# Kernel optimization log

Measured on AMD Instinct MI355X. Metric: run time of the kernel, lower is better.

The kernel has to match this reference:

```python
import jax, jax.numpy as jnp
import numpy as np
import math

B, C, H, W = 16, 256, 128, 128
N = 4096
D = 256  # out_channels
IMG = 512


def _bilinear_sample(features, grid):
    """features (B,C,H,W), grid (B,N,2) in [-1,1] (x,y). align_corners=True, border padding."""
    Bq, Cq, Hq, Wq = features.shape
    ix = (grid[..., 0] + 1.0) * 0.5 * (Wq - 1)  # (B,N)
    iy = (grid[..., 1] + 1.0) * 0.5 * (Hq - 1)
    # border padding: clamp continuous coords into valid range
    ix = jnp.clip(ix, 0.0, Wq - 1)
    iy = jnp.clip(iy, 0.0, Hq - 1)
    x0 = jnp.floor(ix)
    y0 = jnp.floor(iy)
    wx = ix - x0
    wy = iy - y0
    x0i = jnp.clip(x0.astype(jnp.int32), 0, Wq - 1)
    y0i = jnp.clip(y0.astype(jnp.int32), 0, Hq - 1)
    x1i = jnp.clip(x0i + 1, 0, Wq - 1)
    y1i = jnp.clip(y0i + 1, 0, Hq - 1)
    f = features.reshape(Bq, Cq, Hq * Wq)

    def gather(yi, xi):
        idx = (yi * Wq + xi)[:, None, :]  # (B,1,N)
        return jnp.take_along_axis(f, idx, axis=2)  # (B,C,N)

    v00 = gather(y0i, x0i)
    v01 = gather(y0i, x1i)
    v10 = gather(y1i, x0i)
    v11 = gather(y1i, x1i)
    wx = wx[:, None, :]
    wy = wy[:, None, :]
    top = v00 * (1 - wx) + v01 * wx
    bot = v10 * (1 - wx) + v11 * wx
    return top * (1 - wy) + bot * wy  # (B,C,N)


def _pos_encoding(positions, d_model):
    """positions (B,N,2) in [0,1] -> (B,N,2*d_model) sinusoidal."""
    div_term = jnp.exp(jnp.arange(0, d_model, 2, dtype=jnp.float32)
                       * (-math.log(10000.0) / d_model))  # (d_model//2,)
    x = positions[..., 0:1] * 1000.0  # (B,N,1)
    y = positions[..., 1:2] * 1000.0

    def interleave(v):
        a = v * div_term  # (B,N,d_model//2)
        sc = jnp.stack([jnp.sin(a), jnp.cos(a)], axis=-1)  # (B,N,d//2,2)
        return sc.reshape(*v.shape[:-1], d_model)

    return jnp.concatenate([interleave(x), interleave(y)], axis=-1)


def setup_inputs() -> dict:
    key = jax.random.key(0)
    ks = jax.random.split(key, 8)
    features = jax.random.normal(ks[0], (B, C, H, W), dtype=jnp.float32)
    vertices = jax.random.uniform(ks[1], (B, N, 2), dtype=jnp.float32) * IMG
    s1 = 1.0 / math.sqrt(C)
    s2 = 1.0 / math.sqrt(D)
    W1 = jax.random.uniform(ks[2], (C, D), jnp.float32, -s1, s1)
    b1 = jnp.zeros((D,), jnp.float32)
    W2 = jax.random.uniform(ks[3], (D, D), jnp.float32, -s2, s2)
    b2 = jnp.zeros((D,), jnp.float32)
    Wp = jax.random.uniform(ks[4], (D, D), jnp.float32, -s2, s2)
    bp = jnp.zeros((D,), jnp.float32)
    return {"features": features, "vertices": vertices, "image_size": IMG,
            "W1": W1, "b1": b1, "W2": W2, "b2": b2, "Wp": Wp, "bp": bp}


def reference(features, vertices, image_size, W1, b1, W2, b2, Wp, bp):
    # normalize pixel coords to [-1,1] (align_corners=True convention)
    denom = jnp.float32(image_size - 1)
    grid = 2.0 * vertices / denom - 1.0  # (B,N,2)
    sampled = _bilinear_sample(features, grid)  # (B,C,N)
    sampled = jnp.transpose(sampled, (0, 2, 1))  # (B,N,C)
    h = jax.nn.relu(jnp.einsum('bnc,cd->bnd', sampled, W1) + b1)
    vfeat = jnp.einsum('bnd,de->bne', h, W2) + b2  # (B,N,D)
    pos_enc = _pos_encoding(vertices / jnp.float32(image_size), D // 2)  # (B,N,D)
    out = jnp.einsum('bnd,de->bne', vfeat + pos_enc, Wp) + bp
    return out
```

## Files before the change

### kernel.cpp

```cpp
#include <hip/hip_runtime.h>

#define HW 16384
#define Nn 4096

typedef __bf16 bf16x8 __attribute__((ext_vector_type(8)));
typedef unsigned short us8t __attribute__((ext_vector_type(8)));
typedef float f32x4 __attribute__((ext_vector_type(4)));

__device__ __forceinline__ unsigned short f2bf(float f) {
    unsigned int u = __float_as_uint(f);
    u = (u + 0x7fffu + ((u >> 16) & 1u)) >> 16;
    return (unsigned short)u;
}
__device__ __forceinline__ float bf2f(unsigned int h) {
    return __uint_as_float(h << 16);
}
__device__ __forceinline__ f32x4 mfma16(us8t a, us8t b, f32x4 c) {
    return __builtin_amdgcn_mfma_f32_16x16x32_bf16(
        __builtin_bit_cast(bf16x8, a), __builtin_bit_cast(bf16x8, b), c, 0, 0, 0);
}

__global__ __launch_bounds__(256) void k_wt(const float* __restrict__ W1,
                                            const float* __restrict__ W2,
                                            const float* __restrict__ Wp,
                                            unsigned short* __restrict__ WT) {
    const int m = blockIdx.x >> 8;
    const int d = blockIdx.x & 255;
    const int c = threadIdx.x;
    const float* W = (m == 0) ? W1 : (m == 1) ? W2 : Wp;
    WT[m * 65536 + d * 256 + c] = f2bf(W[c * 256 + d]);
}

__global__ __launch_bounds__(256) void k_gemm1(const float* __restrict__ f,
                                               const unsigned short* __restrict__ W1T,
                                               unsigned short* __restrict__ S, int b0) {
    __shared__ __align__(16) unsigned short Asb[64][40];

    const int blk = blockIdx.x;
    const int bl = blk >> 8;
    const int b = b0 + bl;
    const int p0 = (blk & 255) << 6;
    const int t = threadIdx.x;
    const int lane = t & 63;
    const int w = t >> 6;
    const int sc = t >> 4;
    const int sp = (t & 15) << 2;
    const int mrow = lane & 15;
    const int kg = (lane >> 4) << 3;
    const int n0w = w << 6;

    const float* fb = f + ((size_t)b << 22);

    f32x4 acc[4][4];
#pragma unroll
    for (int i = 0; i < 4; ++i)
#pragma unroll
        for (int j = 0; j < 4; ++j) acc[i][j] = (f32x4){0.f, 0.f, 0.f, 0.f};

    us8t bnx[4];
#pragma unroll
    for (int nt = 0; nt < 4; ++nt)
        bnx[nt] = *(const us8t*)(W1T + ((n0w + (nt << 4) + mrow) << 8) + kg);

    for (int k0 = 0; k0 < 256; k0 += 32) {
        __syncthreads();
#pragma unroll
        for (int it = 0; it < 2; ++it) {
            const int c = sc + (it << 4);
            const float4 v = *(const float4*)(fb + ((size_t)(k0 + c) << 14) + p0 + sp);
            Asb[sp + 0][c] = f2bf(v.x);
            Asb[sp + 1][c] = f2bf(v.y);
            Asb[sp + 2][c] = f2bf(v.z);
            Asb[sp + 3][c] = f2bf(v.w);
        }
        us8t bcur[4];
#pragma unroll
        for (int nt = 0; nt < 4; ++nt) bcur[nt] = bnx[nt];
        if (k0 < 224) {
#pragma unroll
            for (int nt = 0; nt < 4; ++nt)
                bnx[nt] = *(const us8t*)(W1T + ((n0w + (nt << 4) + mrow) << 8) + k0 + 32 + kg);
        }
        __syncthreads();
        us8t af[4];
#pragma unroll
        for (int mt = 0; mt < 4; ++mt)
            af[mt] = *(const us8t*)&Asb[(mt << 4) + mrow][kg];
#pragma unroll
        for (int mt = 0; mt < 4; ++mt)
#pragma unroll
            for (int nt = 0; nt < 4; ++nt)
                acc[mt][nt] = mfma16(af[mt], bcur[nt], acc[mt][nt]);
    }

    unsigned short* Sp = S + ((((size_t)bl << 14) + p0) << 8);
    const int r0 = (lane >> 4) << 2;
#pragma unroll
    for (int mt = 0; mt < 4; ++mt)
#pragma unroll
        for (int nt = 0; nt < 4; ++nt) {
            const int col = n0w + (nt << 4) + mrow;
#pragma unroll
            for (int j = 0; j < 4; ++j) {
                const int row = (mt << 4) + r0 + j;
                Sp[((size_t)row << 8) + col] = f2bf(acc[mt][nt][j]);
            }
        }
}

__global__ __launch_bounds__(256) void k_fused(const unsigned short* __restrict__ S,
                                               const float* __restrict__ verts,
                                               const int* __restrict__ iszp,
                                               const unsigned short* __restrict__ W2T,
                                               const unsigned short* __restrict__ WpT,
                                               const float* __restrict__ b1,
                                               const float* __restrict__ b2,
                                               const float* __restrict__ bpv,
                                               float* __restrict__ out, int b0) {
    __shared__ __align__(16) unsigned short hT[64][264];
    __shared__ __align__(16) int pIdx[64][4];
    __shared__ __align__(16) float wBl[64][4];
    __shared__ float vps[64][2];
    __shared__ __align__(16) float b1s[256];
    __shared__ float b2s[256], bps[256];

    const int blk = blockIdx.x;
    const int bl = blk >> 6;
    const int b = b0 + bl;
    const int n0 = (blk & 63) << 6;
    const int t = threadIdx.x;
    const int lane = t & 63;
    const int w = t >> 6;

    b1s[t] = b1[t];
    b2s[t] = b2[t];
    bps[t] = bpv[t];

    if (t < 64) {
        const float isz = (float)iszp[0];
        const size_t vo = ((size_t)b * Nn + n0 + t) << 1;
        const float vx = verts[vo + 0];
        const float vy = verts[vo + 1];
        const float gs = 127.0f / (isz - 1.0f);
        const float ix = fminf(fmaxf(vx * gs, 0.0f), 127.0f);
        const float iy = fminf(fmaxf(vy * gs, 0.0f), 127.0f);
        const float x0 = floorf(ix), y0 = floorf(iy);
        const float wx = ix - x0, wy = iy - y0;
        const int x0i = (int)x0, y0i = (int)y0;
        const int x1i = min(x0i + 1, 127), y1i = min(y0i + 1, 127);
        pIdx[t][0] = (y0i << 7) + x0i;
        pIdx[t][1] = (y0i << 7) + x1i;
        pIdx[t][2] = (y1i << 7) + x0i;
        pIdx[t][3] = (y1i << 7) + x1i;
        wBl[t][0] = (1.0f - wx) * (1.0f - wy);
        wBl[t][1] = wx * (1.0f - wy);
        wBl[t][2] = (1.0f - wx) * wy;
        wBl[t][3] = wx * wy;
        vps[t][0] = vx / isz;
        vps[t][1] = vy / isz;
    }
    __syncthreads();

    {
        const unsigned short* Sb = S + ((size_t)bl << 22);
        const float4 bl1 = *(const float4*)&b1s[lane << 2];
        for (int i = 0; i < 16; ++i) {
            const int r = (w << 4) + i;
            const int4 pp = *(const int4*)pIdx[r];
            const float4 wt = *(const float4*)wBl[r];
            const uint2 a0 = *(const uint2*)(Sb + ((size_t)pp.x << 8) + (lane << 2));
            const uint2 a1 = *(const uint2*)(Sb + ((size_t)pp.y << 8) + (lane << 2));
            const uint2 a2 = *(const uint2*)(Sb + ((size_t)pp.z << 8) + (lane << 2));
            const uint2 a3 = *(const uint2*)(Sb + ((size_t)pp.w << 8) + (lane << 2));
            float d0 = wt.x * bf2f(a0.x & 0xffffu) + wt.y * bf2f(a1.x & 0xffffu) +
                       wt.z * bf2f(a2.x & 0xffffu) + wt.w * bf2f(a3.x & 0xffffu) + bl1.x;
            float d1 = wt.x * bf2f(a0.x >> 16) + wt.y * bf2f(a1.x >> 16) +
                       wt.z * bf2f(a2.x >> 16) + wt.w * bf2f(a3.x >> 16) + bl1.y;
            float d2 = wt.x * bf2f(a0.y & 0xffffu) + wt.y * bf2f(a1.y & 0xffffu) +
                       wt.z * bf2f(a2.y & 0xffffu) + wt.w * bf2f(a3.y & 0xffffu) + bl1.z;
            float d3 = wt.x * bf2f(a0.y >> 16) + wt.y * bf2f(a1.y >> 16) +
                       wt.z * bf2f(a2.y >> 16) + wt.w * bf2f(a3.y >> 16) + bl1.w;
            d0 = fmaxf(d0, 0.0f);
            d1 = fmaxf(d1, 0.0f);
            d2 = fmaxf(d2, 0.0f);
            d3 = fmaxf(d3, 0.0f);
            uint2 pk;
            pk.x = (unsigned)f2bf(d0) | ((unsigned)f2bf(d1) << 16);
            pk.y = (unsigned)f2bf(d2) | ((unsigned)f2bf(d3) << 16);
            *(uint2*)&hT[r][lane << 2] = pk;
        }
    }
    __syncthreads();

    const int mrow = lane & 15;
    const int kg = (lane >> 4) << 3;
    const int r0 = (lane >> 4) << 2;
    const int n0w = w << 6;

    f32x4 acc[4][4];
#pragma unroll
    for (int i = 0; i < 4; ++i)
#pragma unroll
        for (int j = 0; j < 4; ++j) acc[i][j] = (f32x4){0.f, 0.f, 0.f, 0.f};

    us8t bnx[4];
#pragma unroll
    for (int nt = 0; nt < 4; ++nt)
        bnx[nt] = *(const us8t*)(W2T + ((n0w + (nt << 4) + mrow) << 8) + kg);
    for (int k0 = 0; k0 < 256; k0 += 32) {
        us8t bcur[4];
#pragma unroll
        for (int nt = 0; nt < 4; ++nt) bcur[nt] = bnx[nt];
        if (k0 < 224) {
#pragma unroll
            for (int nt = 0; nt < 4; ++nt)
                bnx[nt] = *(const us8t*)(W2T + ((n0w + (nt << 4) + mrow) << 8) + k0 + 32 + kg);
        }
        us8t af[4];
#pragma unroll
        for (int mt = 0; mt < 4; ++mt)
            af[mt] = *(const us8t*)&hT[(mt << 4) + mrow][k0 + kg];
#pragma unroll
        for (int mt = 0; mt < 4; ++mt)
#pragma unroll
            for (int nt = 0; nt < 4; ++nt)
                acc[mt][nt] = mfma16(af[mt], bcur[nt], acc[mt][nt]);
    }
    __syncthreads();

    const float C2 = -0.20762050593046f;
#pragma unroll
    for (int nt = 0; nt < 4; ++nt) {
        const int col = n0w + (nt << 4) + mrow;
        const float bias2 = b2s[col];
        const int ci = col & 127;
        const float dv = exp2f((float)(ci >> 1) * C2) * 1000.0f;
        const int sel = col >> 7;
#pragma unroll
        for (int mt = 0; mt < 4; ++mt)
#pragma unroll
            for (int j = 0; j < 4; ++j) {
                const int row = (mt << 4) + r0 + j;
                const float ang = vps[row][sel] * dv;
                const float pe = (col & 1) ? __cosf(ang) : __sinf(ang);
                hT[row][col] = f2bf(acc[mt][nt][j] + bias2 + pe);
            }
    }
    __syncthreads();

#pragma unroll
    for (int i = 0; i < 4; ++i)
#pragma unroll
        for (int j = 0; j < 4; ++j) acc[i][j] = (f32x4){0.f, 0.f, 0.f, 0.f};
#pragma unroll
    for (int nt = 0; nt < 4; ++nt)
        bnx[nt] = *(const us8t*)(WpT + ((n0w + (nt << 4) + mrow) << 8) + kg);
    for (int k0 = 0; k0 < 256; k0 += 32) {
        us8t bcur[4];
#pragma unroll
        for (int nt = 0; nt < 4; ++nt) bcur[nt] = bnx[nt];
        if (k0 < 224) {
#pragma unroll
            for (int nt = 0; nt < 4; ++nt)
                bnx[nt] = *(const us8t*)(WpT + ((n0w + (nt << 4) + mrow) << 8) + k0 + 32 + kg);
        }
        us8t af[4];
#pragma unroll
        for (int mt = 0; mt < 4; ++mt)
            af[mt] = *(const us8t*)&hT[(mt << 4) + mrow][k0 + kg];
#pragma unroll
        for (int mt = 0; mt < 4; ++mt)
#pragma unroll
            for (int nt = 0; nt < 4; ++nt)
                acc[mt][nt] = mfma16(af[mt], bcur[nt], acc[mt][nt]);
    }

    float* ob = out + (((size_t)b * Nn + n0) << 8);
#pragma unroll
    for (int nt = 0; nt < 4; ++nt) {
        const int col = n0w + (nt << 4) + mrow;
        const float bb = bps[col];
#pragma unroll
        for (int mt = 0; mt < 4; ++mt)
#pragma unroll
            for (int j = 0; j < 4; ++j) {
                const int row = (mt << 4) + r0 + j;
                ob[((size_t)row << 8) + col] = acc[mt][nt][j] + bb;
            }
    }
}

extern "C" void kernel_launch(void* const* d_in, const int* in_sizes, int n_in,
                              void* d_out, int out_size, void* d_ws, size_t ws_size,
                              hipStream_t stream) {
    const float* f = (const float*)d_in[0];
    const float* verts = (const float*)d_in[1];
    const int* isz = (const int*)d_in[2];
    const float* W1 = (const float*)d_in[3];
    const float* b1 = (const float*)d_in[4];
    const float* W2 = (const float*)d_in[5];
    const float* b2 = (const float*)d_in[6];
    const float* Wp = (const float*)d_in[7];
    const float* bp = (const float*)d_in[8];
    float* out = (float*)d_out;

    unsigned short* WT = (unsigned short*)d_ws;
    const size_t S_OFF = 512u << 10;
    unsigned short* S = (unsigned short*)((char*)d_ws + S_OFF);

    const size_t perBatch = (size_t)HW * 256 * 2;
    size_t sbytes = (ws_size > S_OFF) ? (ws_size - S_OFF) : 0;
    int nbMax = (int)(sbytes / perBatch);
    if (nbMax < 1) nbMax = 1;
    if (nbMax > 16) nbMax = 16;

    k_wt<<<dim3(768), dim3(256), 0, stream>>>(W1, W2, Wp, WT);
    for (int b0 = 0; b0 < 16; b0 += nbMax) {
        const int nb = (16 - b0 < nbMax) ? (16 - b0) : nbMax;
        k_gemm1<<<dim3(nb * 256), dim3(256), 0, stream>>>(f, WT, S, b0);
        k_fused<<<dim3(nb * 64), dim3(256), 0, stream>>>(S, verts, isz, WT + 65536, WT + 131072,
                                                         b1, b2, bp, out, b0);
    }
}
```

Before: 515.5 us.

## Split gather from MLP kernel and load all channels up front in pixel GEMM

The pixel-projection GEMM now loads all 256 channels of a 64-pixel tile into LDS in one pass, using packed bf16 conversion, and drops the per-k-step barriers. It also swaps operand roles so the weights feed the MFMA A operand, which allows packed vector stores. The bilinear gather plus ReLU becomes its own kernel with one vertex per wave, writing h to a workspace buffer, and the MLP kernel reads h directly from global memory. This aims to raise gather parallelism and cut synchronisation, at the cost of an extra launch, an h round-trip through memory, and a smaller batch chunk per workspace.

```diff
diff --git a/kernel.cpp b/kernel.cpp
--- a/kernel.cpp
+++ b/kernel.cpp
@@ -6,6 +6,7 @@
 typedef __bf16 bf16x8 __attribute__((ext_vector_type(8)));
 typedef unsigned short us8t __attribute__((ext_vector_type(8)));
 typedef float f32x4 __attribute__((ext_vector_type(4)));
+typedef unsigned int u32x4 __attribute__((ext_vector_type(4)));
 
 __device__ __forceinline__ unsigned short f2bf(float f) {
     unsigned int u = __float_as_uint(f);
@@ -14,6 +15,11 @@
 }
 __device__ __forceinline__ float bf2f(unsigned int h) {
     return __uint_as_float(h << 16);
+}
+__device__ __forceinline__ unsigned int pack2bf(float lo, float hi) {
+    const unsigned int u0 = __float_as_uint(lo) + 0x8000u;
+    const unsigned int u1 = __float_as_uint(hi) + 0x8000u;
+    return __builtin_amdgcn_perm(u1, u0, 0x07060302u);
 }
 __device__ __forceinline__ f32x4 mfma16(us8t a, us8t b, f32x4 c) {
     return __builtin_amdgcn_mfma_f32_16x16x32_bf16(
@@ -31,10 +37,10 @@
     WT[m * 65536 + d * 256 + c] = f2bf(W[c * 256 + d]);
 }
 
-__global__ __launch_bounds__(256) void k_gemm1(const float* __restrict__ f,
-                                               const unsigned short* __restrict__ W1T,
-                                               unsigned short* __restrict__ S, int b0) {
-    __shared__ __align__(16) unsigned short Asb[64][40];
+__global__ __launch_bounds__(256) void k_pix(const float* __restrict__ f,
+                                             const unsigned short* __restrict__ W1T,
+                                             unsigned short* __restrict__ S, int b0) {
+    __shared__ __align__(16) unsigned int Asb[64 * 132];
 
     const int blk = blockIdx.x;
     const int bl = blk >> 8;
@@ -43,85 +49,145 @@
     const int t = threadIdx.x;
     const int lane = t & 63;
     const int w = t >> 6;
-    const int sc = t >> 4;
-    const int sp = (t & 15) << 2;
     const int mrow = lane & 15;
     const int kg = (lane >> 4) << 3;
-    const int n0w = w << 6;
 
     const float* fb = f + ((size_t)b << 22);
 
+    const int sp = (t & 15) << 2;
+    const int c8 = (t >> 4) << 3;
+#pragma unroll
+    for (int pass = 0; pass < 2; ++pass) {
+        const int c0 = c8 + (pass << 7);
+        f32x4 v[8];
+#pragma unroll
+        for (int i = 0; i < 8; ++i)
+            v[i] = *(const f32x4*)(fb + ((size_t)(c0 + i) << 14) + p0 + sp);
+#pragma unroll
+        for (int j = 0; j < 4; ++j) {
+            u32x4 pk;
+            pk.x = pack2bf(v[0][j], v[1][j]);
+            pk.y = pack2bf(v[2][j], v[3][j]);
+            pk.z = pack2bf(v[4][j], v[5][j]);
+            pk.w = pack2bf(v[6][j], v[7][j]);
+            *(u32x4*)&Asb[(sp + j) * 132 + (c0 >> 1)] = pk;
+        }
+    }
+
     f32x4 acc[4][4];
 #pragma unroll
     for (int i = 0; i < 4; ++i)
 #pragma unroll
         for (int j = 0; j < 4; ++j) acc[i][j] = (f32x4){0.f, 0.f, 0.f, 0.f};
 
-    us8t bnx[4];
-#pragma unroll
-    for (int nt = 0; nt < 4; ++nt)
-        bnx[nt] = *(const us8t*)(W1T + ((n0w + (nt << 4) + mrow) << 8) + kg);
-
+    const unsigned short* AW = W1T + (((w << 6) + mrow) << 8) + kg;
+    us8t aN[4];
+#pragma unroll
+    for (int mt = 0; mt < 4; ++mt) aN[mt] = *(const us8t*)(AW + (mt << 12));
+
+    __syncthreads();
+
+    const unsigned short* Bl = (const unsigned short*)Asb + mrow * 264 + kg;
+#pragma unroll
     for (int k0 = 0; k0 < 256; k0 += 32) {
-        __syncthreads();
-#pragma unroll
-        for (int it = 0; it < 2; ++it) {
-            const int c = sc + (it << 4);
-            const float4 v = *(const float4*)(fb + ((size_t)(k0 + c) << 14) + p0 + sp);
-            Asb[sp + 0][c] = f2bf(v.x);
-            Asb[sp + 1][c] = f2bf(v.y);
-            Asb[sp + 2][c] = f2bf(v.z);
-            Asb[sp + 3][c] = f2bf(v.w);
-        }
-        us8t bcur[4];
-#pragma unroll
-        for (int nt = 0; nt < 4; ++nt) bcur[nt] = bnx[nt];
+        us8t aC[4];
+#pragma unroll
+        for (int mt = 0; mt < 4; ++mt) aC[mt] = aN[mt];
         if (k0 < 224) {
 #pragma unroll
+            for (int mt = 0; mt < 4; ++mt)
+                aN[mt] = *(const us8t*)(AW + (mt << 12) + k0 + 32);
+        }
+        us8t bF[4];
+#pragma unroll
+        for (int nt = 0; nt < 4; ++nt)
+            bF[nt] = *(const us8t*)(Bl + nt * 16 * 264 + k0);
+#pragma unroll
+        for (int mt = 0; mt < 4; ++mt)
+#pragma unroll
             for (int nt = 0; nt < 4; ++nt)
-                bnx[nt] = *(const us8t*)(W1T + ((n0w + (nt << 4) + mrow) << 8) + k0 + 32 + kg);
-        }
-        __syncthreads();
-        us8t af[4];
-#pragma unroll
-        for (int mt = 0; mt < 4; ++mt)
-            af[mt] = *(const us8t*)&Asb[(mt << 4) + mrow][kg];
-#pragma unroll
-        for (int mt = 0; mt < 4; ++mt)
-#pragma unroll
-            for (int nt = 0; nt < 4; ++nt)
-                acc[mt][nt] = mfma16(af[mt], bcur[nt], acc[mt][nt]);
-    }
-
-    unsigned short* Sp = S + ((((size_t)bl << 14) + p0) << 8);
-    const int r0 = (lane >> 4) << 2;
-#pragma unroll
-    for (int mt = 0; mt < 4; ++mt)
-#pragma unroll
-        for (int nt = 0; nt < 4; ++nt) {
-            const int col = n0w + (nt << 4) + mrow;
-#pragma unroll
-            for (int j = 0; j < 4; ++j) {
-                const int row = (mt << 4) + r0 + j;
-                Sp[((size_t)row << 8) + col] = f2bf(acc[mt][nt][j]);
-            }
-        }
-}
-
-__global__ __launch_bounds__(256) void k_fused(const unsigned short* __restrict__ S,
-                                               const float* __restrict__ verts,
-                                               const int* __restrict__ iszp,
-                                               const unsigned short* __restrict__ W2T,
-                                               const unsigned short* __restrict__ WpT,
-                                               const float* __restrict__ b1,
-                                               const float* __restrict__ b2,
-                                               const float* __restrict__ bpv,
-                                               float* __restrict__ out, int b0) {
-    __shared__ __align__(16) unsigned short hT[64][264];
-    __shared__ __align__(16) int pIdx[64][4];
-    __shared__ __align__(16) float wBl[64][4];
+                acc[mt][nt] = mfma16(aC[mt], bF[nt], acc[mt][nt]);
+    }
+
+    unsigned short* Sp = S + ((((size_t)bl << 14) + p0 + mrow) << 8) + (w << 6) + ((lane >> 4) << 2);
+#pragma unroll
+    for (int nt = 0; nt < 4; ++nt) {
+        unsigned short* Sr = Sp + ((size_t)(nt << 4) << 8);
+#pragma unroll
+        for (int mt = 0; mt < 4; ++mt) {
+            uint2 pk;
+            pk.x = pack2bf(acc[mt][nt][0], acc[mt][nt][1]);
+            pk.y = pack2bf(acc[mt][nt][2], acc[mt][nt][3]);
+            *(uint2*)(Sr + (mt << 4)) = pk;
+        }
+    }
+}
+
+__global__ __launch_bounds__(256) void k_gather(const unsigned short* __restrict__ S,
+                                                const float* __restrict__ verts,
+                                                const int* __restrict__ iszp,
+                                                const float* __restrict__ b1,
+                                                unsigned short* __restrict__ h, int b0) {
+    const int t = threadIdx.x;
+    const int lane = t & 63;
+    const int w = t >> 6;
+    const int blk = blockIdx.x;
+    const int bl = blk >> 10;
+    const int n = ((blk & 1023) << 2) + w;
+    const int b = b0 + bl;
+
+    const float isz = (float)iszp[0];
+    const size_t vo = ((size_t)b * Nn + n) << 1;
+    const float vx = verts[vo];
+    const float vy = verts[vo + 1];
+    const float gs = 127.0f / (isz - 1.0f);
+    const float ix = fminf(fmaxf(vx * gs, 0.0f), 127.0f);
+    const float iy = fminf(fmaxf(vy * gs, 0.0f), 127.0f);
+    const float x0 = floorf(ix), y0 = floorf(iy);
+    const float wx = ix - x0, wy = iy - y0;
+    const int x0i = (int)x0, y0i = (int)y0;
+    const int x1i = min(x0i + 1, 127), y1i = min(y0i + 1, 127);
+    const float w00 = (1.0f - wx) * (1.0f - wy);
+    const float w01 = wx * (1.0f - wy);
+    const float w10 = (1.0f - wx) * wy;
+    const float w11 = wx * wy;
+
+    const unsigned short* Sb = S + ((size_t)bl << 22);
+    const int co = lane << 2;
+    const uint2 a0 = *(const uint2*)(Sb + (((size_t)(y0i << 7) + x0i) << 8) + co);
+    const uint2 a1 = *(const uint2*)(Sb + (((size_t)(y0i << 7) + x1i) << 8) + co);
+    const uint2 a2 = *(const uint2*)(Sb + (((size_t)(y1i << 7) + x0i) << 8) + co);
+    const uint2 a3 = *(const uint2*)(Sb + (((size_t)(y1i << 7) + x1i) << 8) + co);
+    const float4 bb = *(const float4*)(b1 + co);
+
+    float d0 = w00 * bf2f(a0.x & 0xffffu) + w01 * bf2f(a1.x & 0xffffu) +
+               w10 * bf2f(a2.x & 0xffffu) + w11 * bf2f(a3.x & 0xffffu) + bb.x;
+    float d1 = w00 * bf2f(a0.x >> 16) + w01 * bf2f(a1.x >> 16) +
+               w10 * bf2f(a2.x >> 16) + w11 * bf2f(a3.x >> 16) + bb.y;
+    float d2 = w00 * bf2f(a0.y & 0xffffu) + w01 * bf2f(a1.y & 0xffffu) +
+               w10 * bf2f(a2.y & 0xffffu) + w11 * bf2f(a3.y & 0xffffu) + bb.z;
+    float d3 = w00 * bf2f(a0.y >> 16) + w01 * bf2f(a1.y >> 16) +
+               w10 * bf2f(a2.y >> 16) + w11 * bf2f(a3.y >> 16) + bb.w;
+    d0 = fmaxf(d0, 0.0f);
+    d1 = fmaxf(d1, 0.0f);
+    d2 = fmaxf(d2, 0.0f);
+    d3 = fmaxf(d3, 0.0f);
+    uint2 pk;
+    pk.x = pack2bf(d0, d1);
+    pk.y = pack2bf(d2, d3);
+    *(uint2*)(h + (((size_t)bl * Nn + n) << 8) + co) = pk;
+}
+
+__global__ __launch_bounds__(256) void k_mlp(const unsigned short* __restrict__ h,
+                                             const float* __restrict__ verts,
+                                             const int* __restrict__ iszp,
+                                             const unsigned short* __restrict__ W2T,
+                                             const unsigned short* __restrict__ WpT,
+                                             const float* __restrict__ b2,
+                                             const float* __restrict__ bpv,
+                                             float* __restrict__ out, int b0) {
+    __shared__ __align__(16) unsigned short gT[64][264];
     __shared__ float vps[64][2];
-    __shared__ __align__(16) float b1s[256];
     __shared__ float b2s[256], bps[256];
 
     const int blk = blockIdx.x;
@@ -132,99 +198,49 @@
     const int lane = t & 63;
     const int w = t >> 6;
 
-    b1s[t] = b1[t];
     b2s[t] = b2[t];
     bps[t] = bpv[t];
-
     if (t < 64) {
         const float isz = (float)iszp[0];
         const size_t vo = ((size_t)b * Nn + n0 + t) << 1;
-        const float vx = verts[vo + 0];
-        const float vy = verts[vo + 1];
-        const float gs = 127.0f / (isz - 1.0f);
-        const float ix = fminf(fmaxf(vx * gs, 0.0f), 127.0f);
-        const float iy = fminf(fmaxf(vy * gs, 0.0f), 127.0f);
-        const float x0 = floorf(ix), y0 = floorf(iy);
-        const float wx = ix - x0, wy = iy - y0;
-        const int x0i = (int)x0, y0i = (int)y0;
-        const int x1i = min(x0i + 1, 127), y1i = min(y0i + 1, 127);
-        pIdx[t][0] = (y0i << 7) + x0i;
-        pIdx[t][1] = (y0i << 7) + x1i;
-        pIdx[t][2] = (y1i << 7) + x0i;
-        pIdx[t][3] = (y1i << 7) + x1i;
-        wBl[t][0] = (1.0f - wx) * (1.0f - wy);
-        wBl[t][1] = wx * (1.0f - wy);
-        wBl[t][2] = (1.0f - wx) * wy;
-        wBl[t][3] = wx * wy;
-        vps[t][0] = vx / isz;
-        vps[t][1] = vy / isz;
-    }
-    __syncthreads();
-
-    {
-        const unsigned short* Sb = S + ((size_t)bl << 22);
-        const float4 bl1 = *(const float4*)&b1s[lane << 2];
-        for (int i = 0; i < 16; ++i) {
-            const int r = (w << 4) + i;
-            const int4 pp = *(const int4*)pIdx[r];
-            const float4 wt = *(const float4*)wBl[r];
-            const uint2 a0 = *(const uint2*)(Sb + ((size_t)pp.x << 8) + (lane << 2));
-            const uint2 a1 = *(const uint2*)(Sb + ((size_t)pp.y << 8) + (lane << 2));
-            const uint2 a2 = *(const uint2*)(Sb + ((size_t)pp.z << 8) + (lane << 2));
-            const uint2 a3 = *(const uint2*)(Sb + ((size_t)pp.w << 8) + (lane << 2));
-            float d0 = wt.x * bf2f(a0.x & 0xffffu) + wt.y * bf2f(a1.x & 0xffffu) +
-                       wt.z * bf2f(a2.x & 0xffffu) + wt.w * bf2f(a3.x & 0xffffu) + bl1.x;
-            float d1 = wt.x * bf2f(a0.x >> 16) + wt.y * bf2f(a1.x >> 16) +
-                       wt.z * bf2f(a2.x >> 16) + wt.w * bf2f(a3.x >> 16) + bl1.y;
-            float d2 = wt.x * bf2f(a0.y & 0xffffu) + wt.y * bf2f(a1.y & 0xffffu) +
-                       wt.z * bf2f(a2.y & 0xffffu) + wt.w * bf2f(a3.y & 0xffffu) + bl1.z;
-            float d3 = wt.x * bf2f(a0.y >> 16) + wt.y * bf2f(a1.y >> 16) +
-                       wt.z * bf2f(a2.y >> 16) + wt.w * bf2f(a3.y >> 16) + bl1.w;
-            d0 = fmaxf(d0, 0.0f);
-            d1 = fmaxf(d1, 0.0f);
-            d2 = fmaxf(d2, 0.0f);
-            d3 = fmaxf(d3, 0.0f);
-            uint2 pk;
-            pk.x = (unsigned)f2bf(d0) | ((unsigned)f2bf(d1) << 16);
-            pk.y = (unsigned)f2bf(d2) | ((unsigned)f2bf(d3) << 16);
-            *(uint2*)&hT[r][lane << 2] = pk;
-        }
-    }
-    __syncthreads();
+        vps[t][0] = verts[vo] / isz;
+        vps[t][1] = verts[vo + 1] / isz;
+    }
 
     const int mrow = lane & 15;
     const int kg = (lane >> 4) << 3;
     const int r0 = (lane >> 4) << 2;
     const int n0w = w << 6;
 
+    const unsigned short* hb = h + (((size_t)bl * Nn + n0 + mrow) << 8) + kg;
+    const unsigned short* B2 = W2T + ((n0w + mrow) << 8) + kg;
     f32x4 acc[4][4];
 #pragma unroll
     for (int i = 0; i < 4; ++i)
 #pragma unroll
         for (int j = 0; j < 4; ++j) acc[i][j] = (f32x4){0.f, 0.f, 0.f, 0.f};
 
-    us8t bnx[4];
-#pragma unroll
-    for (int nt = 0; nt < 4; ++nt)
-        bnx[nt] = *(const us8t*)(W2T + ((n0w + (nt << 4) + mrow) << 8) + kg);
+    us8t aN[4], bN[4];
+#pragma unroll
+    for (int mt = 0; mt < 4; ++mt) aN[mt] = *(const us8t*)(hb + (mt << 12));
+#pragma unroll
+    for (int nt = 0; nt < 4; ++nt) bN[nt] = *(const us8t*)(B2 + (nt << 12));
+#pragma unroll
     for (int k0 = 0; k0 < 256; k0 += 32) {
-        us8t bcur[4];
-#pragma unroll
-        for (int nt = 0; nt < 4; ++nt) bcur[nt] = bnx[nt];
+        us8t aC[4], bC[4];
+#pragma unroll
+        for (int i = 0; i < 4; ++i) { aC[i] = aN[i]; bC[i] = bN[i]; }
         if (k0 < 224) {
 #pragma unroll
+            for (int mt = 0; mt < 4; ++mt) aN[mt] = *(const us8t*)(hb + (mt << 12) + k0 + 32);
+#pragma unroll
+            for (int nt = 0; nt < 4; ++nt) bN[nt] = *(const us8t*)(B2 + (nt << 12) + k0 + 32);
+        }
+#pragma unroll
+        for (int mt = 0; mt < 4; ++mt)
+#pragma unroll
             for (int nt = 0; nt < 4; ++nt)
-                bnx[nt] = *(const us8t*)(W2T + ((n0w + (nt << 4) + mrow) << 8) + k0 + 32 + kg);
-        }
-        us8t af[4];
-#pragma unroll
-        for (int mt = 0; mt < 4; ++mt)
-            af[mt] = *(const us8t*)&hT[(mt << 4) + mrow][k0 + kg];
-#pragma unroll
-        for (int mt = 0; mt < 4; ++mt)
-#pragma unroll
-            for (int nt = 0; nt < 4; ++nt)
-                acc[mt][nt] = mfma16(af[mt], bcur[nt], acc[mt][nt]);
+                acc[mt][nt] = mfma16(aC[mt], bC[nt], acc[mt][nt]);
     }
     __syncthreads();
 
@@ -243,7 +259,8 @@
                 const int row = (mt << 4) + r0 + j;
                 const float ang = vps[row][sel] * dv;
                 const float pe = (col & 1) ? __cosf(ang) : __sinf(ang);
-                hT[row][col] = f2bf(acc[mt][nt][j] + bias2 + pe);
+                const float val = acc[mt][nt][j] + bias2 + pe;
+                gT[row][col] = (unsigned short)((__float_as_uint(val) + 0x8000u) >> 16);
             }
     }
     __syncthreads();
@@ -252,27 +269,28 @@
     for (int i = 0; i < 4; ++i)
 #pragma unroll
         for (int j = 0; j < 4; ++j) acc[i][j] = (f32x4){0.f, 0.f, 0.f, 0.f};
-#pragma unroll
-    for (int nt = 0; nt < 4; ++nt)
-        bnx[nt] = *(const us8t*)(WpT + ((n0w + (nt << 4) + mrow) << 8) + kg);
+    const unsigned short* Bp = WpT + ((n0w + mrow) << 8) + kg;
+#pragma unroll
+    for (int nt = 0; nt < 4; ++nt) bN[nt] = *(const us8t*)(Bp + (nt << 12));
+    const unsigned short* Al = &gT[mrow][kg];
+#pragma unroll
     for (int k0 = 0; k0 < 256; k0 += 32) {
-        us8t bcur[4];
-#pragma unroll
-        for (int nt = 0; nt < 4; ++nt) bcur[nt] = bnx[nt];
+        us8t bC[4];
+#pragma unroll
+        for (int i = 0; i < 4; ++i) bC[i] = bN[i];
         if (k0 < 224) {
 #pragma unroll
+            for (int nt = 0; nt < 4; ++nt) bN[nt] = *(const us8t*)(Bp + (nt << 12) + k0 + 32);
+        }
+        us8t aC[4];
+#pragma unroll
+        for (int mt = 0; mt < 4; ++mt)
+            aC[mt] = *(const us8t*)(Al + mt * 16 * 264 + k0);
+#pragma unroll
+        for (int mt = 0; mt < 4; ++mt)
+#pragma unroll
             for (int nt = 0; nt < 4; ++nt)
-                bnx[nt] = *(const us8t*)(WpT + ((n0w + (nt << 4) + mrow) << 8) + k0 + 32 + kg);
-        }
-        us8t af[4];
-#pragma unroll
-        for (int mt = 0; mt < 4; ++mt)
-            af[mt] = *(const us8t*)&hT[(mt << 4) + mrow][k0 + kg];
-#pragma unroll
-        for (int mt = 0; mt < 4; ++mt)
-#pragma unroll
-            for (int nt = 0; nt < 4; ++nt)
-                acc[mt][nt] = mfma16(af[mt], bcur[nt], acc[mt][nt]);
+                acc[mt][nt] = mfma16(aC[mt], bC[nt], acc[mt][nt]);
     }
 
     float* ob = out + (((size_t)b * Nn + n0) << 8);
@@ -305,20 +323,22 @@
     float* out = (float*)d_out;
 
     unsigned short* WT = (unsigned short*)d_ws;
-    const size_t S_OFF = 512u << 10;
-    unsigned short* S = (unsigned short*)((char*)d_ws + S_OFF);
-
-    const size_t perBatch = (size_t)HW * 256 * 2;
-    size_t sbytes = (ws_size > S_OFF) ? (ws_size - S_OFF) : 0;
-    int nbMax = (int)(sbytes / perBatch);
+    const size_t S_OFF = 1u << 20;
+    const size_t perS = (size_t)HW * 256 * 2;
+    const size_t perH = (size_t)Nn * 256 * 2;
+    const size_t avail = (ws_size > S_OFF) ? (ws_size - S_OFF) : 0;
+    int nbMax = (int)(avail / (perS + perH));
     if (nbMax < 1) nbMax = 1;
     if (nbMax > 16) nbMax = 16;
+    unsigned short* S = (unsigned short*)((char*)d_ws + S_OFF);
+    unsigned short* Hb = (unsigned short*)((char*)d_ws + S_OFF + (size_t)nbMax * perS);
 
     k_wt<<<dim3(768), dim3(256), 0, stream>>>(W1, W2, Wp, WT);
     for (int b0 = 0; b0 < 16; b0 += nbMax) {
         const int nb = (16 - b0 < nbMax) ? (16 - b0) : nbMax;
-        k_gemm1<<<dim3(nb * 256), dim3(256), 0, stream>>>(f, WT, S, b0);
-        k_fused<<<dim3(nb * 64), dim3(256), 0, stream>>>(S, verts, isz, WT + 65536, WT + 131072,
-                                                         b1, b2, bp, out, b0);
-    }
-}
+        k_pix<<<dim3(nb * 256), dim3(256), 0, stream>>>(f, WT, S, b0);
+        k_gather<<<dim3(nb * 1024), dim3(256), 0, stream>>>(S, verts, isz, b1, Hb, b0);
+        k_mlp<<<dim3(nb * 64), dim3(256), 0, stream>>>(Hb, verts, isz, WT + 65536, WT + 131072,
+                                                       b2, bp, out, b0);
+    }
+}
```

Result: slower. 539.4 us (+4.7%).
